# Optimization experiments

Measured on AMD Instinct MI355X. Metric: run time of the kernel, lower is better.

## Reference

```python
import jax, jax.numpy as jnp
import numpy as np

L = 13   # num hidden states (embeddings + 12 layers)
B = 32   # batch
N = 512  # sequence length
H = 768  # per-layer hidden size
M = 384  # mapping_size = embed_size // downsample_D_factor
E = 768  # embed_size


def setup_inputs() -> dict:
    key = jax.random.key(0)
    ks = jax.random.split(key, 8)
    s = 0.02
    return {
        "all_hidden_features": jax.random.normal(ks[0], (L, B, N, H), jnp.float32),
        "lengths": jax.random.randint(ks[1], (B,), 1, N + 1),  # valid lengths in [1, N]
        "W_down": jax.random.normal(ks[2], (L, H, M), jnp.float32) * s,
        "b_down": jnp.zeros((L, M), jnp.float32),
        "g_down": jnp.ones((L, M), jnp.float32),
        "beta_down": jnp.zeros((L, M), jnp.float32),
        "W_proj": jax.random.normal(ks[3], (M, M), jnp.float32) * s,
        "b_proj": jnp.zeros((M,), jnp.float32),
        "g_proj": jnp.ones((M,), jnp.float32),
        "beta_proj": jnp.zeros((M,), jnp.float32),
        "W_up": jax.random.normal(ks[4], (M, E), jnp.float32) * s,
        "b_up": jnp.zeros((E,), jnp.float32),
        "W_gate": jax.random.normal(ks[5], (M, 1), jnp.float32) * s,
        "b_gate": jnp.zeros((1,), jnp.float32),
    }


def _ln(x, g, b, eps=1e-5):
    mu = jnp.mean(x, axis=-1, keepdims=True)
    var = jnp.var(x, axis=-1, keepdims=True)
    return (x - mu) * jax.lax.rsqrt(var + eps) * g + b


def reference(all_hidden_features, lengths, W_down, b_down, g_down, beta_down,
              W_proj, b_proj, g_proj, beta_proj, W_up, b_up, W_gate, b_gate):
    # mask: [B, N] 1.0 for valid positions
    mask = (jnp.arange(N)[None, :] < lengths[:, None]).astype(jnp.float32)

    # per-layer downsample: Linear + LayerNorm over all L layers at once -> [L, B, N, M]
    down = _ln(jnp.einsum('lbnh,lhm->lbnm', all_hidden_features, W_down)
               + b_down[:, None, None, :],
               g_down[:, None, None, :], beta_down[:, None, None, :])

    anchor_feat = down[-1]                      # [B, N, M]
    denom = jnp.sum(mask, axis=1)[:, None]      # [B, 1]
    anchor = jnp.sum(anchor_feat * mask[:, :, None], axis=1) / denom  # [B, M]

    targets = down[:-1]                         # [L-1, B, N, M]
    t_agg = jnp.sum(targets * mask[None, :, :, None], axis=2) / denom[None]  # [L-1, B, M]

    # cross-attention: relu + L1-normalized weights + identity, mask on context dim
    cw = jnp.einsum('bnm,lbkm->lbnk', anchor_feat, targets)  # [L-1, B, N, N]
    cw = jax.nn.relu(cw * mask[None, :, None, :])
    cw = cw / (jnp.sum(cw, axis=-1, keepdims=True) + 1e-8) + jnp.eye(N, dtype=cw.dtype)
    merged = jnp.einsum('lbnk,lbkm->lbnm', cw, targets)      # [L-1, B, N, M]

    # gated fusion across layers
    logits = (jnp.einsum('lbm,mo->lbo', anchor[None] * t_agg, W_gate) + b_gate)[..., 0]  # [L-1, B]
    conf = jax.nn.softmax(logits.T, axis=1)                  # [B, L-1]
    msum = jnp.einsum('lbnm,bl->bnm', merged, conf)          # [B, N, M]

    out = anchor_feat + _ln(msum @ W_proj + b_proj, g_proj, beta_proj)
    return (jax.nn.relu(out) @ W_up + b_up, lengths)
```

## Files before the change

### kernel.cpp

```cpp
#include <hip/hip_runtime.h>

#define LL 13
#define BB 32
#define NN 512
#define HH 768
#define MM 384
#define EE 768
#define BN (BB*NN)
#define K12 (12*NN)

typedef __attribute__((ext_vector_type(8))) short s16x8;
typedef __attribute__((ext_vector_type(4))) float f32x4;
typedef unsigned int u32;
#define AS1 __attribute__((address_space(1)))
#define AS3 __attribute__((address_space(3)))

__device__ __forceinline__ short f2bf(float f) {
    union { float f; u32 u; } c; c.f = f;
    u32 u = c.u;
    return (short)((u + 0x7fffu + ((u >> 16) & 1u)) >> 16);
}
__device__ __forceinline__ float bf2f(short h) {
    union { u32 u; float f; } c; c.u = ((u32)(unsigned short)h) << 16;
    return c.f;
}
__device__ __forceinline__ void gload16(const void* g, void* l) {
    __builtin_amdgcn_global_load_lds((const AS1 u32*)g, (AS3 u32*)l, 16, 0, 0);
}

template<bool AFP32>
__device__ __forceinline__ void gemm_core(const char* At, int lda,
                                          const char* Bt, int ldb,
                                          int K, char* lds, f32x4 acc[4][4])
{
    const int tid  = threadIdx.x;
    const int lane = tid & 63;
    const int w    = tid >> 6;
    const int mt0 = (w >> 1) * 4;
    const int nt0 = (w & 1) * 4;

    const int rg0 = (w*2)*16 + (lane & 15);
    const int rg1 = rg0 + 16;
    const int kcb = (lane >> 4) * 16;
    const char* gb0 = Bt + (size_t)rg0 * ldb * 2 + kcb;
    const char* gb1 = Bt + (size_t)rg1 * ldb * 2 + kcb;
    const int lboff0 = 8192 + (w*2)*1024;
    const int lboff1 = lboff0 + 1024;

    auto mfma_step = [&](int bo) {
        s16x8 af[4], bf4[4];
        char* sA = lds + bo;
        char* sB = sA + 8192;
        #pragma unroll
        for (int i = 0; i < 4; ++i) af[i] = *(const s16x8*)(sA + ((mt0+i)<<10) + lane*16);
        #pragma unroll
        for (int j = 0; j < 4; ++j) bf4[j] = *(const s16x8*)(sB + ((nt0+j)<<10) + lane*16);
        #pragma unroll
        for (int i = 0; i < 4; ++i)
            #pragma unroll
            for (int j = 0; j < 4; ++j)
                acc[i][j] = __builtin_amdgcn_mfma_f32_16x16x32_bf16(af[i], bf4[j], acc[i][j], 0, 0, 0);
    };

    if (!AFP32) {
        const char* ga0 = At + (size_t)rg0 * lda * 2 + kcb;
        const char* ga1 = At + (size_t)rg1 * lda * 2 + kcb;
        const int laoff0 = (w*2)*1024, laoff1 = laoff0 + 1024;
        gload16(ga0, lds + laoff0); gload16(ga1, lds + laoff1);
        gload16(gb0, lds + lboff0); gload16(gb1, lds + lboff1);
        ga0 += 64; ga1 += 64; gb0 += 64; gb1 += 64;
        __syncthreads();
        int bo = 0;
        for (int k0 = 32; k0 < K; k0 += 32) {
            const int nbo = bo ^ 16384;
            gload16(ga0, lds + nbo + laoff0); gload16(ga1, lds + nbo + laoff1);
            gload16(gb0, lds + nbo + lboff0); gload16(gb1, lds + nbo + lboff1);
            ga0 += 64; ga1 += 64; gb0 += 64; gb1 += 64;
            mfma_step(bo);
            __syncthreads();
            bo = nbo;
        }
        mfma_step(bo);
    } else {
        size_t goff_[4]; int loff_[4];
        #pragma unroll
        for (int c = 0; c < 4; ++c) {
            int id = c*256 + tid;
            int row = id >> 3, c16 = id & 7;
            goff_[c] = (size_t)row * lda * 4 + c16 * 16;
            loff_[c] = ((row>>4)*64 + (row&15) + (c16>>1)*16)*16 + (c16&1)*8;
        }
        f32x4 g[4];
        #pragma unroll
        for (int c = 0; c < 4; ++c) g[c] = *(const f32x4*)(At + goff_[c]);
        gload16(gb0, lds + lboff0); gload16(gb1, lds + lboff1);
        gb0 += 64; gb1 += 64;
        #pragma unroll
        for (int c = 0; c < 4; ++c) {
            u32 p0 = ((u32)(unsigned short)f2bf(g[c][0])) | (((u32)(unsigned short)f2bf(g[c][1])) << 16);
            u32 p1 = ((u32)(unsigned short)f2bf(g[c][2])) | (((u32)(unsigned short)f2bf(g[c][3])) << 16);
            u32* d = (u32*)(lds + loff_[c]);
            d[0] = p0; d[1] = p1;
        }
        __syncthreads();
        int bo = 0;
        size_t kb = 128;
        for (int k0 = 32; k0 < K; k0 += 32, kb += 128) {
            const int nbo = bo ^ 16384;
            #pragma unroll
            for (int c = 0; c < 4; ++c) g[c] = *(const f32x4*)(At + goff_[c] + kb);
            gload16(gb0, lds + nbo + lboff0); gload16(gb1, lds + nbo + lboff1);
            gb0 += 64; gb1 += 64;
            mfma_step(bo);
            #pragma unroll
            for (int c = 0; c < 4; ++c) {
                u32 p0 = ((u32)(unsigned short)f2bf(g[c][0])) | (((u32)(unsigned short)f2bf(g[c][1])) << 16);
                u32 p1 = ((u32)(unsigned short)f2bf(g[c][2])) | (((u32)(unsigned short)f2bf(g[c][3])) << 16);
                u32* d = (u32*)(lds + nbo + loff_[c]);
                d[0] = p0; d[1] = p1;
            }
            __syncthreads();
            bo = nbo;
        }
        mfma_step(bo);
    }
}

__device__ __forceinline__ void zero_acc(f32x4 acc[4][4]) {
    #pragma unroll
    for (int i = 0; i < 4; ++i)
        #pragma unroll
        for (int j = 0; j < 4; ++j) {
            acc[i][j][0] = 0.f; acc[i][j][1] = 0.f;
            acc[i][j][2] = 0.f; acc[i][j][3] = 0.f;
        }
}

__global__ __launch_bounds__(256) void k_wt(const float* __restrict__ in, short* __restrict__ out,
                                            int R, int C, size_t zin, size_t zout)
{
    __shared__ short L[64][80];
    const float* I = in + (size_t)blockIdx.z * zin;
    short* O = out + (size_t)blockIdx.z * zout;
    const int r0 = blockIdx.y * 64, c0 = blockIdx.x * 64;
    const int t = threadIdx.x;
    {
        int r = t >> 2, cq = (t & 3) * 16;
        const float* p = I + (size_t)(r0 + r) * C + c0 + cq;
        s16x8 a, b;
        f32x4 u0 = *(const f32x4*)(p);
        f32x4 u1 = *(const f32x4*)(p + 4);
        f32x4 u2 = *(const f32x4*)(p + 8);
        f32x4 u3 = *(const f32x4*)(p + 12);
        a[0]=f2bf(u0[0]); a[1]=f2bf(u0[1]); a[2]=f2bf(u0[2]); a[3]=f2bf(u0[3]);
        a[4]=f2bf(u1[0]); a[5]=f2bf(u1[1]); a[6]=f2bf(u1[2]); a[7]=f2bf(u1[3]);
        b[0]=f2bf(u2[0]); b[1]=f2bf(u2[1]); b[2]=f2bf(u2[2]); b[3]=f2bf(u2[3]);
        b[4]=f2bf(u3[0]); b[5]=f2bf(u3[1]); b[6]=f2bf(u3[2]); b[7]=f2bf(u3[3]);
        *(s16x8*)&L[r][cq]     = a;
        *(s16x8*)&L[r][cq + 8] = b;
    }
    __syncthreads();
    #pragma unroll
    for (int it = 0; it < 2; ++it) {
        int id = it * 256 + t;
        int cc = id >> 3, rq = id & 7;
        s16x8 v;
        #pragma unroll
        for (int e = 0; e < 8; ++e) v[e] = L[rq*8 + e][cc];
        *(s16x8*)(O + (size_t)(c0 + cc) * R + r0 + rq*8) = v;
    }
}

__global__ __launch_bounds__(256) void k_down(const float* __restrict__ X,
                                              const short* __restrict__ WdT,
                                              const float* __restrict__ bd,
                                              short* __restrict__ down)
{
    __shared__ char lds[36864];
    const int lg = ((blockIdx.x & 7) * 624) + (blockIdx.x >> 3);
    const int col0 = (lg % 3) * 128;
    const int row0 = ((lg / 3) & 127) * 128;
    const int l = lg / 384;
    const char* At = (const char*)(X   + (size_t)l*BN*HH + (size_t)row0*HH);
    const char* Bt = (const char*)(WdT + (size_t)l*MM*HH + (size_t)col0*HH);
    f32x4 acc[4][4]; zero_acc(acc);
    gemm_core<true>(At, HH, Bt, HH, HH, lds, acc);

    const int tid = threadIdx.x, lane = tid & 63, w = tid >> 6;
    const int wr = w >> 1, wc = w & 1;
    float bj[4];
    #pragma unroll
    for (int j = 0; j < 4; ++j) bj[j] = bd[l*MM + col0 + wc*64 + j*16 + (lane & 15)];
    __syncthreads();
    short* ep = (short*)(lds + w * 9216);
    #pragma unroll
    for (int i = 0; i < 4; ++i) {
        int rr = i*16 + (lane >> 4) * 4;
        #pragma unroll
        for (int j = 0; j < 4; ++j) {
            int cc = j*16 + (lane & 15);
            #pragma unroll
            for (int r = 0; r < 4; ++r)
                ep[(rr + r)*72 + cc] = f2bf(acc[i][j][r] + bj[j]);
        }
    }
    __syncthreads();
    short* C = down + (size_t)l*BN*MM;
    #pragma unroll
    for (int it = 0; it < 8; ++it) {
        int c = it*64 + lane;
        int row = c >> 3, kq = c & 7;
        s16x8 v = *(const s16x8*)(ep + row*72 + kq*8);
        int grow = row0 + wr*64 + row;
        int gcol = col0 + wc*64 + kq*8;
        *(s16x8*)(C + (size_t)grow*MM + gcol) = v;
    }
}

__global__ __launch_bounds__(256) void k_ln(short* __restrict__ down,
                                            const float* __restrict__ g,
                                            const float* __restrict__ beta,
                                            short* __restrict__ downTb)
{
    __shared__ short Lt[64][392];
    const int blk = blockIdx.x;
    const int l = blk / (BB*8);
    const int rem = blk % (BB*8);
    const int b = rem >> 3;
    const int n0 = (rem & 7) * 64;
    const int tid = threadIdx.x, lane = tid & 63, w = tid >> 6;

    for (int it = 0; it < 16; ++it) {
        int ri = it*4 + w;
        int n = n0 + ri;
        short* p = down + (((size_t)l*BB + b)*NN + n) * MM;
        float v[6]; float s = 0.f, s2 = 0.f;
        #pragma unroll
        for (int t = 0; t < 6; ++t) { v[t] = bf2f(p[lane + t*64]); s += v[t]; s2 += v[t]*v[t]; }
        #pragma unroll
        for (int off = 32; off; off >>= 1) { s += __shfl_xor(s, off); s2 += __shfl_xor(s2, off); }
        float mu  = s * (1.f/MM);
        float inv = rsqrtf(s2 * (1.f/MM) - mu*mu + 1e-5f);
        #pragma unroll
        for (int t = 0; t < 6; ++t) {
            int m = lane + t*64;
            short o = f2bf((v[t]-mu)*inv * g[l*MM + m] + beta[l*MM + m]);
            p[m] = o;
            Lt[ri][m] = o;
        }
    }
    if (l == 12) return;
    __syncthreads();
    short* O = downTb + ((size_t)b*MM*12 + l) * NN;
    #pragma unroll
    for (int it = 0; it < 12; ++it) {
        int id = it*256 + tid;
        int m = id >> 3, nq = id & 7;
        s16x8 vv;
        #pragma unroll
        for (int e = 0; e < 8; ++e) vv[e] = Lt[nq*8 + e][m];
        *(s16x8*)(O + (size_t)m*12*NN + n0 + nq*8) = vv;
    }
}

__global__ __launch_bounds__(384) void k_agg(const short* __restrict__ down,
                                             const int* __restrict__ lengths,
                                             float* __restrict__ t_agg,
                                             float* __restrict__ anchor)
{
    const int b = blockIdx.x;
    const int l = blockIdx.y;
    const int m = threadIdx.x;
    const int len = lengths[b];
    const short* p = down + ((size_t)l*BB + b)*NN*MM;
    float s = 0.f;
    for (int n = 0; n < len; ++n) s += bf2f(p[(size_t)n*MM + m]);
    s /= (float)len;
    if (l == 12) anchor[b*MM + m] = s;
    else         t_agg[((size_t)l*BB + b)*MM + m] = s;
}

__global__ __launch_bounds__(64) void k_conf(const float* __restrict__ anchor,
                                             const float* __restrict__ t_agg,
                                             const float* __restrict__ Wg,
                                             const float* __restrict__ bg,
                                             float* __restrict__ conf)
{
    const int b = blockIdx.x;
    const int lane = threadIdx.x;
    float lg[12];
    #pragma unroll
    for (int l = 0; l < 12; ++l) {
        float s = 0.f;
        #pragma unroll
        for (int t = 0; t < 6; ++t) {
            int m = lane + t*64;
            s += anchor[b*MM + m] * t_agg[((size_t)l*BB + b)*MM + m] * Wg[m];
        }
        #pragma unroll
        for (int off = 32; off; off >>= 1) s += __shfl_xor(s, off);
        lg[l] = s + bg[0];
    }
    float mx = lg[0];
    #pragma unroll
    for (int l = 1; l < 12; ++l) mx = fmaxf(mx, lg[l]);
    float den = 0.f, e[12];
    #pragma unroll
    for (int l = 0; l < 12; ++l) { e[l] = expf(lg[l]-mx); den += e[l]; }
    if (lane == 0) {
        #pragma unroll
        for (int l = 0; l < 12; ++l) conf[b*12 + l] = e[l]/den;
    }
}

__global__ __launch_bounds__(256) void k_s(const short* __restrict__ down,
                                           const int* __restrict__ lengths,
                                           short* __restrict__ cw)
{
    __shared__ char lds[36864];
    const int lg = ((blockIdx.x & 7) * 768) + (blockIdx.x >> 3);
    const int col0 = (lg & 3) * 128;
    const int row0 = ((lg >> 2) & 3) * 128;
    const int z = lg >> 4;
    const int b = z / 12;
    const int l = z % 12;
    const char* At = (const char*)(down + ((size_t)12*BB + b)*NN*MM + (size_t)row0*MM);
    const char* Bt = (const char*)(down + ((size_t)l*BB  + b)*NN*MM + (size_t)col0*MM);
    f32x4 acc[4][4]; zero_acc(acc);
    gemm_core<false>(At, MM, Bt, MM, MM, lds, acc);

    const int tid = threadIdx.x, lane = tid & 63, w = tid >> 6;
    const int wr = w >> 1, wc = w & 1;
    const int len = lengths[b];
    __syncthreads();
    short* ep = (short*)(lds + w * 9216);
    #pragma unroll
    for (int i = 0; i < 4; ++i) {
        int rr = i*16 + (lane >> 4) * 4;
        #pragma unroll
        for (int j = 0; j < 4; ++j) {
            int cc = j*16 + (lane & 15);
            bool keep = (col0 + wc*64 + cc) < len;
            #pragma unroll
            for (int r = 0; r < 4; ++r) {
                float v = keep ? fmaxf(acc[i][j][r], 0.f) : 0.f;
                ep[(rr + r)*72 + cc] = f2bf(v);
            }
        }
    }
    __syncthreads();
    short* C = cw + ((size_t)b*NN + row0 + wr*64)*K12 + (size_t)l*NN + col0 + wc*64;
    #pragma unroll
    for (int it = 0; it < 8; ++it) {
        int c = it*64 + lane;
        int row = c >> 3, kq = c & 7;
        s16x8 v = *(const s16x8*)(ep + row*72 + kq*8);
        *(s16x8*)(C + (size_t)row*K12 + kq*8) = v;
    }
}

__global__ __launch_bounds__(256) void k_norm(short* __restrict__ cw,
                                              const float* __restrict__ conf)
{
    const int rid  = blockIdx.x*4 + (threadIdx.x >> 6);
    const int lane = threadIdx.x & 63;
    const int b   = rid / (NN*12);
    const int rem = rid % (NN*12);
    const int n   = rem / 12;
    const int l   = rem % 12;
    short* p = cw + ((size_t)b*NN + n)*K12 + (size_t)l*NN + lane*8;
    s16x8 v = *(const s16x8*)p;
    float f[8]; float s = 0.f;
    #pragma unroll
    for (int e = 0; e < 8; ++e) { f[e] = bf2f(v[e]); s += f[e]; }
    #pragma unroll
    for (int off = 32; off; off >>= 1) s += __shfl_xor(s, off);
    const float cf = conf[b*12 + l];
    const float sc = cf / (s + 1e-8f);
    #pragma unroll
    for (int e = 0; e < 8; ++e) {
        float o = f[e] * sc;
        if (lane*8 + e == n) o += cf;
        v[e] = f2bf(o);
    }
    *(s16x8*)p = v;
}

__global__ __launch_bounds__(256) void k_merge(const short* __restrict__ cw,
                                               const short* __restrict__ downTb,
                                               short* __restrict__ msum)
{
    __shared__ char lds[36864];
    const int lg = ((blockIdx.x & 7) * 48) + (blockIdx.x >> 3);
    const int col0 = (lg % 3) * 128;
    const int row0 = ((lg / 3) & 3) * 128;
    const int b = lg / 12;
    const char* At = (const char*)(cw     + ((size_t)b*NN + row0)*K12);
    const char* Bt = (const char*)(downTb + ((size_t)b*MM + col0)*K12);
    f32x4 acc[4][4]; zero_acc(acc);
    gemm_core<false>(At, K12, Bt, K12, K12, lds, acc);

    const int tid = threadIdx.x, lane = tid & 63, w = tid >> 6;
    const int wr = w >> 1, wc = w & 1;
    __syncthreads();
    short* ep = (short*)(lds + w * 9216);
    #pragma unroll
    for (int i = 0; i < 4; ++i) {
        int rr = i*16 + (lane >> 4) * 4;
        #pragma unroll
        for (int j = 0; j < 4; ++j) {
            int cc = j*16 + (lane & 15);
            #pragma unroll
            for (int r = 0; r < 4; ++r)
                ep[(rr + r)*72 + cc] = f2bf(acc[i][j][r]);
        }
    }
    __syncthreads();
    short* C = msum + ((size_t)b*NN + row0 + wr*64)*MM + col0 + wc*64;
    #pragma unroll
    for (int it = 0; it < 8; ++it) {
        int c = it*64 + lane;
        int row = c >> 3, kq = c & 7;
        s16x8 v = *(const s16x8*)(ep + row*72 + kq*8);
        *(s16x8*)(C + (size_t)row*MM + kq*8) = v;
    }
}

__global__ __launch_bounds__(256) void k_proj(const short* __restrict__ msum,
                                              const short* __restrict__ WpT,
                                              const float* __restrict__ bp,
                                              float* __restrict__ tmp)
{
    __shared__ char lds[32768];
    const int lg = ((blockIdx.x & 7) * 48) + (blockIdx.x >> 3);
    const int col0 = (lg % 3) * 128;
    const int row0 = (lg / 3) * 128;
    const char* At = (const char*)(msum + (size_t)row0*MM);
    const char* Bt = (const char*)(WpT + (size_t)col0*MM);
    f32x4 acc[4][4]; zero_acc(acc);
    gemm_core<false>(At, MM, Bt, MM, MM, lds, acc);

    const int tid = threadIdx.x, lane = tid & 63, w = tid >> 6;
    const int wr = w >> 1, wc = w & 1;
    float bj[4];
    #pragma unroll
    for (int j = 0; j < 4; ++j) bj[j] = bp[col0 + wc*64 + j*16 + (lane & 15)];
    #pragma unroll
    for (int i = 0; i < 4; ++i)
        #pragma unroll
        for (int r = 0; r < 4; ++r) {
            int grow = row0 + wr*64 + i*16 + (lane >> 4)*4 + r;
            #pragma unroll
            for (int j = 0; j < 4; ++j) {
                int gcol = col0 + wc*64 + j*16 + (lane & 15);
                tmp[(size_t)grow*MM + gcol] = acc[i][j][r] + bj[j];
            }
        }
}

__global__ __launch_bounds__(256) void k_ln2(const float* __restrict__ tmp,
                                             const short* __restrict__ down,
                                             const float* __restrict__ g,
                                             const float* __restrict__ beta,
                                             short* __restrict__ R)
{
    const int row  = blockIdx.x*4 + (threadIdx.x >> 6);
    const int lane = threadIdx.x & 63;
    const float* p = tmp + (size_t)row*MM;
    const short* af = down + (size_t)12*BN*MM + (size_t)row*MM;
    float v[6]; float s = 0.f, s2 = 0.f;
    #pragma unroll
    for (int t = 0; t < 6; ++t) { v[t] = p[lane + t*64]; s += v[t]; s2 += v[t]*v[t]; }
    #pragma unroll
    for (int off = 32; off; off >>= 1) { s += __shfl_xor(s, off); s2 += __shfl_xor(s2, off); }
    float mu  = s * (1.f/MM);
    float inv = rsqrtf(s2 * (1.f/MM) - mu*mu + 1e-5f);
    #pragma unroll
    for (int t = 0; t < 6; ++t) {
        int m = lane + t*64;
        float o = bf2f(af[m]) + (v[t]-mu)*inv * g[m] + beta[m];
        R[(size_t)row*MM + m] = f2bf(fmaxf(o, 0.f));
    }
}

__global__ __launch_bounds__(256) void k_up(const short* __restrict__ R,
                                            const short* __restrict__ WuT,
                                            const float* __restrict__ bu,
                                            float* __restrict__ Y)
{
    __shared__ char lds[32768];
    const int lg = ((blockIdx.x & 7) * 96) + (blockIdx.x >> 3);
    const int col0 = (lg % 6) * 128;
    const int row0 = (lg / 6) * 128;
    const char* At = (const char*)(R + (size_t)row0*MM);
    const char* Bt = (const char*)(WuT + (size_t)col0*MM);
    f32x4 acc[4][4]; zero_acc(acc);
    gemm_core<false>(At, MM, Bt, MM, MM, lds, acc);

    const int tid = threadIdx.x, lane = tid & 63, w = tid >> 6;
    const int wr = w >> 1, wc = w & 1;
    float bj[4];
    #pragma unroll
    for (int j = 0; j < 4; ++j) bj[j] = bu[col0 + wc*64 + j*16 + (lane & 15)];
    #pragma unroll
    for (int i = 0; i < 4; ++i)
        #pragma unroll
        for (int r = 0; r < 4; ++r) {
            int grow = row0 + wr*64 + i*16 + (lane >> 4)*4 + r;
            #pragma unroll
            for (int j = 0; j < 4; ++j) {
                int gcol = col0 + wc*64 + j*16 + (lane & 15);
                Y[(size_t)grow*EE + gcol] = acc[i][j][r] + bj[j];
            }
        }
}

__global__ void k_len(const int* __restrict__ lengths, float* __restrict__ out)
{
    if (threadIdx.x < BB)
        out[(size_t)BB*NN*EE + threadIdx.x] = (float)lengths[threadIdx.x];
}

extern "C" void kernel_launch(void* const* d_in, const int* in_sizes, int n_in,
                              void* d_out, int out_size, void* d_ws, size_t ws_size,
                              hipStream_t stream)
{
    const float* X    = (const float*)d_in[0];
    const int*   len  = (const int*)  d_in[1];
    const float* Wd   = (const float*)d_in[2];
    const float* bd   = (const float*)d_in[3];
    const float* gd   = (const float*)d_in[4];
    const float* betd = (const float*)d_in[5];
    const float* Wp   = (const float*)d_in[6];
    const float* bp   = (const float*)d_in[7];
    const float* gp   = (const float*)d_in[8];
    const float* betp = (const float*)d_in[9];
    const float* Wu   = (const float*)d_in[10];
    const float* bu   = (const float*)d_in[11];
    const float* Wg   = (const float*)d_in[12];
    const float* bg   = (const float*)d_in[13];
    float* out = (float*)d_out;

    float* ws     = (float*)d_ws;
    float* tmp    = ws;
    float* t_agg  = tmp + 6291456;
    float* anchor = t_agg + 147456;
    float* conf   = anchor + 12288;
    short* down   = (short*)(conf + 384);
    short* downTb = down   + (size_t)81788928;
    short* cw     = downTb + (size_t)75497472;
    short* msum   = cw     + (size_t)100663296;
    short* R      = msum   + (size_t)6291456;
    short* WdT    = R      + (size_t)6291456;
    short* WpT    = WdT    + (size_t)3833856;
    short* WuT    = WpT    + (size_t)147456;

    k_wt<<<dim3(6, 12, 13), 256, 0, stream>>>(Wd, WdT, HH, MM, (size_t)HH*MM, (size_t)HH*MM);
    k_wt<<<dim3(6, 6, 1),   256, 0, stream>>>(Wp, WpT, MM, MM, 0, 0);
    k_wt<<<dim3(12, 6, 1),  256, 0, stream>>>(Wu, WuT, MM, EE, 0, 0);
    k_down<<<4992, 256, 0, stream>>>(X, WdT, bd, down);
    k_ln<<<LL*BB*8, 256, 0, stream>>>(down, gd, betd, downTb);
    k_agg<<<dim3(BB, LL), 384, 0, stream>>>(down, len, t_agg, anchor);
    k_conf<<<BB, 64, 0, stream>>>(anchor, t_agg, Wg, bg, conf);
    k_s<<<6144, 256, 0, stream>>>(down, len, cw);
    k_norm<<<(BB*12*NN)/4, 256, 0, stream>>>(cw, conf);
    k_merge<<<384, 256, 0, stream>>>(cw, downTb, msum);
    k_proj<<<384, 256, 0, stream>>>(msum, WpT, bp, tmp);
    k_ln2<<<BN/4, 256, 0, stream>>>(tmp, down, gp, betp, R);
    k_up<<<768, 256, 0, stream>>>(R, WuT, bu, out);
    k_len<<<1, 64, 0, stream>>>(len, out);
}
```

Baseline: 1.074 ms.

## Split merge GEMM over K halves, use hardware bf16 converts, vectorize LN/agg loads

Several changes at once. The software round-to-nearest bf16 conversion is replaced with the packed hardware instruction v_cvt_pk_bf16_f32 in every kernel. The merge GEMM is split into two K halves to double its block count (384 to 768), with fp32 partials written out and summed by a new reduction kernel. k_ln and k_agg switch to 32-bit paired bf16 loads. The split-K adds extra fp32 traffic and a kernel launch in exchange for better occupancy across the CUs.

```diff
diff --git a/kernel.cpp b/kernel.cpp
--- a/kernel.cpp
+++ b/kernel.cpp
@@ -11,14 +11,18 @@
 
 typedef __attribute__((ext_vector_type(8))) short s16x8;
 typedef __attribute__((ext_vector_type(4))) float f32x4;
+typedef __attribute__((ext_vector_type(4))) unsigned int u32x4;
 typedef unsigned int u32;
 #define AS1 __attribute__((address_space(1)))
 #define AS3 __attribute__((address_space(3)))
 
-__device__ __forceinline__ short f2bf(float f) {
-    union { float f; u32 u; } c; c.f = f;
-    u32 u = c.u;
-    return (short)((u + 0x7fffu + ((u >> 16) & 1u)) >> 16);
+__device__ __forceinline__ u32 cvtpk2(float a, float b) {
+    u32 r; asm("v_cvt_pk_bf16_f32 %0, %1, %2" : "=v"(r) : "v"(a), "v"(b));
+    return r;
+}
+__device__ __forceinline__ short f2bf_hw(float f) {
+    u32 r; asm("v_cvt_pk_bf16_f32 %0, %1, %2" : "=v"(r) : "v"(f), "v"(f));
+    return (short)r;
 }
 __device__ __forceinline__ float bf2f(short h) {
     union { u32 u; float f; } c; c.u = ((u32)(unsigned short)h) << 16;
@@ -97,10 +101,9 @@
         gb0 += 64; gb1 += 64;
         #pragma unroll
         for (int c = 0; c < 4; ++c) {
-            u32 p0 = ((u32)(unsigned short)f2bf(g[c][0])) | (((u32)(unsigned short)f2bf(g[c][1])) << 16);
-            u32 p1 = ((u32)(unsigned short)f2bf(g[c][2])) | (((u32)(unsigned short)f2bf(g[c][3])) << 16);
             u32* d = (u32*)(lds + loff_[c]);
-            d[0] = p0; d[1] = p1;
+            d[0] = cvtpk2(g[c][0], g[c][1]);
+            d[1] = cvtpk2(g[c][2], g[c][3]);
         }
         __syncthreads();
         int bo = 0;
@@ -114,10 +117,9 @@
             mfma_step(bo);
             #pragma unroll
             for (int c = 0; c < 4; ++c) {
-                u32 p0 = ((u32)(unsigned short)f2bf(g[c][0])) | (((u32)(unsigned short)f2bf(g[c][1])) << 16);
-                u32 p1 = ((u32)(unsigned short)f2bf(g[c][2])) | (((u32)(unsigned short)f2bf(g[c][3])) << 16);
                 u32* d = (u32*)(lds + nbo + loff_[c]);
-                d[0] = p0; d[1] = p1;
+                d[0] = cvtpk2(g[c][0], g[c][1]);
+                d[1] = cvtpk2(g[c][2], g[c][3]);
             }
             __syncthreads();
             bo = nbo;
@@ -147,17 +149,17 @@
     {
         int r = t >> 2, cq = (t & 3) * 16;
         const float* p = I + (size_t)(r0 + r) * C + c0 + cq;
-        s16x8 a, b;
         f32x4 u0 = *(const f32x4*)(p);
         f32x4 u1 = *(const f32x4*)(p + 4);
         f32x4 u2 = *(const f32x4*)(p + 8);
         f32x4 u3 = *(const f32x4*)(p + 12);
-        a[0]=f2bf(u0[0]); a[1]=f2bf(u0[1]); a[2]=f2bf(u0[2]); a[3]=f2bf(u0[3]);
-        a[4]=f2bf(u1[0]); a[5]=f2bf(u1[1]); a[6]=f2bf(u1[2]); a[7]=f2bf(u1[3]);
-        b[0]=f2bf(u2[0]); b[1]=f2bf(u2[1]); b[2]=f2bf(u2[2]); b[3]=f2bf(u2[3]);
-        b[4]=f2bf(u3[0]); b[5]=f2bf(u3[1]); b[6]=f2bf(u3[2]); b[7]=f2bf(u3[3]);
-        *(s16x8*)&L[r][cq]     = a;
-        *(s16x8*)&L[r][cq + 8] = b;
+        u32x4 pa, pb;
+        pa[0]=cvtpk2(u0[0],u0[1]); pa[1]=cvtpk2(u0[2],u0[3]);
+        pa[2]=cvtpk2(u1[0],u1[1]); pa[3]=cvtpk2(u1[2],u1[3]);
+        pb[0]=cvtpk2(u2[0],u2[1]); pb[1]=cvtpk2(u2[2],u2[3]);
+        pb[2]=cvtpk2(u3[0],u3[1]); pb[3]=cvtpk2(u3[2],u3[3]);
+        *(u32x4*)&L[r][cq]     = pa;
+        *(u32x4*)&L[r][cq + 8] = pb;
     }
     __syncthreads();
     #pragma unroll
@@ -201,7 +203,7 @@
             int cc = j*16 + (lane & 15);
             #pragma unroll
             for (int r = 0; r < 4; ++r)
-                ep[(rr + r)*72 + cc] = f2bf(acc[i][j][r] + bj[j]);
+                ep[(rr + r)*72 + cc] = f2bf_hw(acc[i][j][r] + bj[j]);
         }
     }
     __syncthreads();
@@ -234,19 +236,28 @@
         int ri = it*4 + w;
         int n = n0 + ri;
         short* p = down + (((size_t)l*BB + b)*NN + n) * MM;
-        float v[6]; float s = 0.f, s2 = 0.f;
-        #pragma unroll
-        for (int t = 0; t < 6; ++t) { v[t] = bf2f(p[lane + t*64]); s += v[t]; s2 += v[t]*v[t]; }
+        u32* pu = (u32*)p;
+        float f[6]; float s = 0.f, s2 = 0.f;
+        #pragma unroll
+        for (int t = 0; t < 3; ++t) {
+            u32 q = pu[lane + t*64];
+            float lo = bf2f((short)(q & 0xffff));
+            float hi = bf2f((short)(q >> 16));
+            f[2*t] = lo; f[2*t+1] = hi;
+            s += lo + hi; s2 += lo*lo + hi*hi;
+        }
         #pragma unroll
         for (int off = 32; off; off >>= 1) { s += __shfl_xor(s, off); s2 += __shfl_xor(s2, off); }
         float mu  = s * (1.f/MM);
         float inv = rsqrtf(s2 * (1.f/MM) - mu*mu + 1e-5f);
         #pragma unroll
-        for (int t = 0; t < 6; ++t) {
-            int m = lane + t*64;
-            short o = f2bf((v[t]-mu)*inv * g[l*MM + m] + beta[l*MM + m]);
-            p[m] = o;
-            Lt[ri][m] = o;
+        for (int t = 0; t < 3; ++t) {
+            int m0 = (lane + t*64) * 2;
+            float o0 = (f[2*t]  -mu)*inv * g[l*MM + m0]     + beta[l*MM + m0];
+            float o1 = (f[2*t+1]-mu)*inv * g[l*MM + m0 + 1] + beta[l*MM + m0 + 1];
+            u32 pk = cvtpk2(o0, o1);
+            pu[lane + t*64] = pk;
+            ((u32*)&Lt[ri][0])[lane + t*64] = pk;
         }
     }
     if (l == 12) return;
@@ -263,21 +274,27 @@
     }
 }
 
-__global__ __launch_bounds__(384) void k_agg(const short* __restrict__ down,
+__global__ __launch_bounds__(192) void k_agg(const short* __restrict__ down,
                                              const int* __restrict__ lengths,
                                              float* __restrict__ t_agg,
                                              float* __restrict__ anchor)
 {
     const int b = blockIdx.x;
     const int l = blockIdx.y;
-    const int m = threadIdx.x;
+    const int c = threadIdx.x;
     const int len = lengths[b];
-    const short* p = down + ((size_t)l*BB + b)*NN*MM;
-    float s = 0.f;
-    for (int n = 0; n < len; ++n) s += bf2f(p[(size_t)n*MM + m]);
-    s /= (float)len;
-    if (l == 12) anchor[b*MM + m] = s;
-    else         t_agg[((size_t)l*BB + b)*MM + m] = s;
+    const u32* base = (const u32*)(down + ((size_t)l*BB + b)*NN*MM);
+    float s0 = 0.f, s1 = 0.f;
+    for (int n = 0; n < len; ++n) {
+        u32 q = base[(size_t)n*192 + c];
+        s0 += bf2f((short)(q & 0xffff));
+        s1 += bf2f((short)(q >> 16));
+    }
+    float inv = 1.f / (float)len;
+    s0 *= inv; s1 *= inv;
+    float* dst = (l == 12) ? (anchor + b*MM) : (t_agg + ((size_t)l*BB + b)*MM);
+    dst[2*c]   = s0;
+    dst[2*c+1] = s1;
 }
 
 __global__ __launch_bounds__(64) void k_conf(const float* __restrict__ anchor,
@@ -344,7 +361,7 @@
             #pragma unroll
             for (int r = 0; r < 4; ++r) {
                 float v = keep ? fmaxf(acc[i][j][r], 0.f) : 0.f;
-                ep[(rr + r)*72 + cc] = f2bf(v);
+                ep[(rr + r)*72 + cc] = f2bf_hw(v);
             }
         }
     }
@@ -381,49 +398,59 @@
     for (int e = 0; e < 8; ++e) {
         float o = f[e] * sc;
         if (lane*8 + e == n) o += cf;
-        v[e] = f2bf(o);
+        v[e] = f2bf_hw(o);
     }
     *(s16x8*)p = v;
 }
 
 __global__ __launch_bounds__(256) void k_merge(const short* __restrict__ cw,
                                                const short* __restrict__ downTb,
-                                               short* __restrict__ msum)
+                                               float* __restrict__ msA,
+                                               float* __restrict__ msB)
 {
     __shared__ char lds[36864];
-    const int lg = ((blockIdx.x & 7) * 48) + (blockIdx.x >> 3);
+    const int lg = ((blockIdx.x & 7) * 96) + (blockIdx.x >> 3);
     const int col0 = (lg % 3) * 128;
     const int row0 = ((lg / 3) & 3) * 128;
-    const int b = lg / 12;
-    const char* At = (const char*)(cw     + ((size_t)b*NN + row0)*K12);
-    const char* Bt = (const char*)(downTb + ((size_t)b*MM + col0)*K12);
+    const int bkh = lg / 12;
+    const int b  = bkh >> 1;
+    const int kh = bkh & 1;
+    const char* At = (const char*)(cw     + ((size_t)b*NN + row0)*K12 + kh*3072);
+    const char* Bt = (const char*)(downTb + ((size_t)b*MM + col0)*K12 + kh*3072);
     f32x4 acc[4][4]; zero_acc(acc);
-    gemm_core<false>(At, K12, Bt, K12, K12, lds, acc);
+    gemm_core<false>(At, K12, Bt, K12, 3072, lds, acc);
 
     const int tid = threadIdx.x, lane = tid & 63, w = tid >> 6;
     const int wr = w >> 1, wc = w & 1;
-    __syncthreads();
-    short* ep = (short*)(lds + w * 9216);
-    #pragma unroll
-    for (int i = 0; i < 4; ++i) {
-        int rr = i*16 + (lane >> 4) * 4;
-        #pragma unroll
-        for (int j = 0; j < 4; ++j) {
-            int cc = j*16 + (lane & 15);
-            #pragma unroll
-            for (int r = 0; r < 4; ++r)
-                ep[(rr + r)*72 + cc] = f2bf(acc[i][j][r]);
-        }
-    }
-    __syncthreads();
-    short* C = msum + ((size_t)b*NN + row0 + wr*64)*MM + col0 + wc*64;
-    #pragma unroll
-    for (int it = 0; it < 8; ++it) {
-        int c = it*64 + lane;
-        int row = c >> 3, kq = c & 7;
-        s16x8 v = *(const s16x8*)(ep + row*72 + kq*8);
-        *(s16x8*)(C + (size_t)row*MM + kq*8) = v;
-    }
+    float* msH = kh ? msB : msA;
+    #pragma unroll
+    for (int i = 0; i < 4; ++i)
+        #pragma unroll
+        for (int r = 0; r < 4; ++r) {
+            int grow = row0 + wr*64 + i*16 + (lane >> 4)*4 + r;
+            #pragma unroll
+            for (int j = 0; j < 4; ++j) {
+                int gcol = col0 + wc*64 + j*16 + (lane & 15);
+                msH[((size_t)b*NN + grow)*MM + gcol] = acc[i][j][r];
+            }
+        }
+}
+
+__global__ __launch_bounds__(256) void k_msum2(const float* __restrict__ msA,
+                                               const float* __restrict__ msB,
+                                               short* __restrict__ msum)
+{
+    size_t i8 = ((size_t)blockIdx.x*256 + threadIdx.x) * 8;
+    f32x4 a0 = *(const f32x4*)(msA + i8);
+    f32x4 a1 = *(const f32x4*)(msA + i8 + 4);
+    f32x4 b0 = *(const f32x4*)(msB + i8);
+    f32x4 b1 = *(const f32x4*)(msB + i8 + 4);
+    u32x4 o;
+    o[0] = cvtpk2(a0[0]+b0[0], a0[1]+b0[1]);
+    o[1] = cvtpk2(a0[2]+b0[2], a0[3]+b0[3]);
+    o[2] = cvtpk2(a1[0]+b1[0], a1[1]+b1[1]);
+    o[3] = cvtpk2(a1[2]+b1[2], a1[3]+b1[3]);
+    *(u32x4*)(msum + i8) = o;
 }
 
 __global__ __launch_bounds__(256) void k_proj(const short* __restrict__ msum,
@@ -479,7 +506,7 @@
     for (int t = 0; t < 6; ++t) {
         int m = lane + t*64;
         float o = bf2f(af[m]) + (v[t]-mu)*inv * g[m] + beta[m];
-        R[(size_t)row*MM + m] = f2bf(fmaxf(o, 0.f));
+        R[(size_t)row*MM + m] = f2bf_hw(fmaxf(o, 0.f));
     }
 }
 
@@ -554,17 +581,20 @@
     short* WdT    = R      + (size_t)6291456;
     short* WpT    = WdT    + (size_t)3833856;
     short* WuT    = WpT    + (size_t)147456;
+    float* msA    = (float*)(WuT + 294912);
+    float* msB    = msA + 6291456;
 
     k_wt<<<dim3(6, 12, 13), 256, 0, stream>>>(Wd, WdT, HH, MM, (size_t)HH*MM, (size_t)HH*MM);
     k_wt<<<dim3(6, 6, 1),   256, 0, stream>>>(Wp, WpT, MM, MM, 0, 0);
     k_wt<<<dim3(12, 6, 1),  256, 0, stream>>>(Wu, WuT, MM, EE, 0, 0);
     k_down<<<4992, 256, 0, stream>>>(X, WdT, bd, down);
     k_ln<<<LL*BB*8, 256, 0, stream>>>(down, gd, betd, downTb);
-    k_agg<<<dim3(BB, LL), 384, 0, stream>>>(down, len, t_agg, anchor);
+    k_agg<<<dim3(BB, LL), 192, 0, stream>>>(down, len, t_agg, anchor);
     k_conf<<<BB, 64, 0, stream>>>(anchor, t_agg, Wg, bg, conf);
     k_s<<<6144, 256, 0, stream>>>(down, len, cw);
     k_norm<<<(BB*12*NN)/4, 256, 0, stream>>>(cw, conf);
-    k_merge<<<384, 256, 0, stream>>>(cw, downTb, msum);
+    k_merge<<<768, 256, 0, stream>>>(cw, downTb, msA, msB);
+    k_msum2<<<3072, 256, 0, stream>>>(msA, msB, msum);
     k_proj<<<384, 256, 0, stream>>>(msum, WpT, bp, tmp);
     k_ln2<<<BN/4, 256, 0, stream>>>(tmp, down, gp, betp, R);
     k_up<<<768, 256, 0, stream>>>(R, WuT, bu, out);
```

Measured after the change: 1.068 ms. About the same (-0.6%).
